# Performance work log

Measured on AMD Instinct MI355X. Metric: run time of the kernel, lower is better.

## Reference

```python
import jax, jax.numpy as jnp
import numpy as np

N_CRYST = 256   # number of crystals
A = 64          # atoms per crystal (uniform)
K = 20          # max_neighbors
HID = 128       # hidden_dim (emb_size_atom/edge)
LAT = 256       # latent_dim
NRBF = 128      # radial basis size
NBLK = 3        # interaction blocks
CUTOFF = 6.0    # radius
N_ATOMS = N_CRYST * A
E = N_ATOMS * K


def _lattice(lengths, angles):
    # lengths, angles: (N_cryst, 3); angles in degrees -> (N_cryst, 3, 3) row-vector lattice
    rad = angles * (np.pi / 180.0)
    cos = jnp.cos(rad)
    sg = jnp.sin(rad[:, 2])
    a, b, c = lengths[:, 0], lengths[:, 1], lengths[:, 2]
    cx = c * cos[:, 1]
    cy = c * (cos[:, 0] - cos[:, 1] * cos[:, 2]) / sg
    cz = jnp.sqrt(jnp.maximum(c ** 2 - cx ** 2 - cy ** 2, 1e-8))
    zeros = jnp.zeros_like(a)
    v1 = jnp.stack([a, zeros, zeros], -1)
    v2 = jnp.stack([b * cos[:, 2], b * sg, zeros], -1)
    v3 = jnp.stack([cx, cy, cz], -1)
    return jnp.stack([v1, v2, v3], axis=1)


def setup_inputs() -> dict:
    key = jax.random.key(0)
    ks = jax.random.split(key, 20)
    z = jax.random.normal(ks[0], (N_CRYST, LAT), jnp.float32)
    frac_coords = jax.random.uniform(ks[1], (N_ATOMS, 3), jnp.float32)
    lengths = 5.0 + 10.0 * jax.random.uniform(ks[2], (N_CRYST, 3), jnp.float32)
    angles = 60.0 + 60.0 * jax.random.uniform(ks[3], (N_CRYST, 3), jnp.float32)
    atom_types = jax.random.randint(ks[4], (N_ATOMS,), 1, 101)
    src = jnp.repeat(jnp.arange(N_ATOMS), K)
    dst = (src // A) * A + jax.random.randint(ks[5], (E,), 0, A)

    def w(k, shape, fan):
        return jax.random.normal(k, shape, jnp.float32) / np.sqrt(fan)

    params = dict(
        emb_table=w(ks[6], (101, HID), 1.0),
        W_in=w(ks[7], (HID + LAT, HID), HID + LAT), b_in=jnp.zeros((HID,), jnp.float32),
        W_edge=w(ks[8], (2 * HID + NRBF, HID), 2 * HID + NRBF), b_edge=jnp.zeros((HID,), jnp.float32),
        Wb_rbf=w(ks[9], (NBLK, NRBF, HID), NRBF),
        Wb_msg=w(ks[10], (NBLK, HID, HID), HID), bb_msg=jnp.zeros((NBLK, HID), jnp.float32),
        Wb_atom=w(ks[11], (NBLK, HID, HID), HID), bb_atom=jnp.zeros((NBLK, HID), jnp.float32),
        Wb_upd=w(ks[12], (NBLK, 3 * HID, HID), 3 * HID), bb_upd=jnp.zeros((NBLK, HID), jnp.float32),
        W_force=w(ks[13], (HID, 1), HID), b_force=jnp.zeros((1,), jnp.float32),
        W_fc1=w(ks[14], (HID, HID), HID), b_fc1=jnp.zeros((HID,), jnp.float32),
        W_fc2=w(ks[15], (HID, HID), HID), b_fc2=jnp.zeros((HID,), jnp.float32),
        W_fc3=w(ks[16], (HID, 2), HID), b_fc3=jnp.zeros((2,), jnp.float32),
    )
    return dict(z=z, frac_coords=frac_coords, lengths=lengths, angles=angles,
                atom_types=atom_types, src=src, dst=dst, **params)


def reference(z, frac_coords, lengths, angles,
              emb_table, W_in, b_in, W_edge, b_edge,
              Wb_rbf, Wb_msg, bb_msg, Wb_atom, bb_atom, Wb_upd, bb_upd,
              W_force, b_force, W_fc1, b_fc1, W_fc2, b_fc2, W_fc3, b_fc3,
              atom_types, src, dst):
    batch_idx = jnp.arange(N_ATOMS) // A  # crystal id per atom
    lattice = _lattice(lengths, angles)   # (N_cryst,3,3)
    cart = jnp.einsum('ni,nij->nj', frac_coords, lattice[batch_idx])  # (N_atoms,3)

    dvec = cart[dst] - cart[src]                        # (E,3)
    dist = jnp.sqrt(jnp.sum(dvec * dvec, -1) + 1e-12)    # (E,)
    unit = dvec / dist[:, None]

    mu = jnp.linspace(0.0, CUTOFF, NRBF)
    delta = CUTOFF / (NRBF - 1)
    env = 0.5 * (jnp.cos(np.pi * jnp.minimum(dist / CUTOFF, 1.0)) + 1.0)  # smooth cutoff
    rbf = jnp.exp(-(((dist[:, None] - mu) / delta) ** 2)) * env[:, None]   # (E,NRBF)

    # atom embedding conditioned on per-crystal latent
    h = jax.nn.relu(jnp.concatenate([emb_table[atom_types], z[batch_idx]], -1) @ W_in + b_in)
    # edge embedding
    m = jax.nn.relu(jnp.concatenate([h[src], h[dst], rbf], -1) @ W_edge + b_edge)

    for i in range(NBLK):
        gate = rbf @ Wb_rbf[i]                                   # (E,HID)
        msg = jax.nn.relu(m @ Wb_msg[i] + bb_msg[i]) * gate       # (E,HID)
        agg = jax.ops.segment_sum(msg, dst, num_segments=N_ATOMS) # (N_atoms,HID)
        h = h + jax.nn.relu(agg @ Wb_atom[i] + bb_atom[i])
        m = m + jax.nn.relu(jnp.concatenate([h[src], h[dst], m], -1) @ Wb_upd[i] + bb_upd[i])

    # per-edge force magnitude projected along edge direction, summed per atom
    f = m @ W_force + b_force                                     # (E,1)
    pred_cart_coord_diff = jax.ops.segment_sum(f * unit, dst, num_segments=N_ATOMS)  # (N_atoms,3)

    a1 = jax.nn.relu(h @ W_fc1 + b_fc1)
    a2 = jax.nn.relu(a1 @ W_fc2 + b_fc2)
    pred_atom_types = a2 @ W_fc3 + b_fc3                          # (N_atoms,2)
    return pred_cart_coord_diff, pred_atom_types
```

## Files before the change

kernel.cpp:

```cpp
#include <hip/hip_runtime.h>
#include <hip/hip_bf16.h>

#define NCRYST 256
#define AATOMS 64
#define KNBR   20
#define HID    128
#define LAT    256
#define NRBF   128
#define NBLK   3
#define NATOMS (NCRYST * AATOMS)
#define NEDGE  (NATOMS * KNBR)
#define NPART  8
#define DQ     4096
#define PI_F   3.14159265358979323846f
#define CUT_F  6.0f
#define CHB    1040
#define EUPGRID 512

typedef short short8 __attribute__((ext_vector_type(8)));
typedef float f32x4  __attribute__((ext_vector_type(4)));

__device__ __forceinline__ float bf2f(__hip_bfloat16 x) { return __bfloat162float(x); }
__device__ __forceinline__ __hip_bfloat16 f2bf(float x) { return __float2bfloat16(x); }
__device__ __forceinline__ float s2f(short x) {
  return __uint_as_float(((unsigned)(unsigned short)x) << 16);
}
__device__ __forceinline__ short f2s(float x) {
  union { short s; __hip_bfloat16 b; } u; u.b = f2bf(x); return u.s;
}

#define DMA16(gptr, lptr) __builtin_amdgcn_global_load_lds( \
    (const __attribute__((address_space(1))) void*)(gptr),  \
    (__attribute__((address_space(3))) void*)(lptr), 16, 0, 0)

#define WCNT_VM11_LGKM0 0x007B
#define WCNT_VM10_LGKM0 0x007A
#define WCNT_VM4_LGKM0  0x0074
#define WCNT_VM0_LGKM0  0x0070
#define WCNT_LGKM0_ONLY 0xC07F

__global__ void k_cart(const float* __restrict__ frac, const float* __restrict__ lengths,
                       const float* __restrict__ angles, float* __restrict__ cart) {
  int atom = blockIdx.x * blockDim.x + threadIdx.x;
  if (atom >= NATOMS) return;
  int c = atom >> 6;
  float al = angles[c*3+0] * (PI_F/180.f);
  float be = angles[c*3+1] * (PI_F/180.f);
  float ga = angles[c*3+2] * (PI_F/180.f);
  float ca = cosf(al), cb = cosf(be), cg = cosf(ga), sg = sinf(ga);
  float a = lengths[c*3+0], b = lengths[c*3+1], cl = lengths[c*3+2];
  float cx = cl * cb;
  float cy = cl * (ca - cb*cg) / sg;
  float cz = sqrtf(fmaxf(cl*cl - cx*cx - cy*cy, 1e-8f));
  float f0 = frac[atom*3+0], f1 = frac[atom*3+1], f2 = frac[atom*3+2];
  cart[atom*3+0] = f0*a + f1*(b*cg) + f2*cx;
  cart[atom*3+1] = f1*(b*sg) + f2*cy;
  cart[atom*3+2] = f2*cz;
}

__global__ void k_edge(const float* __restrict__ cart, const int* __restrict__ src,
                       const int* __restrict__ dst, float* __restrict__ unit,
                       float* __restrict__ dist, const float* __restrict__ b_force,
                       float* __restrict__ fbuf) {
  int e = blockIdx.x * blockDim.x + threadIdx.x;
  if (e >= NEDGE) return;
  int s = src[e], d = dst[e];
  float dx = cart[d*3+0] - cart[s*3+0];
  float dy = cart[d*3+1] - cart[s*3+1];
  float dz = cart[d*3+2] - cart[s*3+2];
  float dd = sqrtf(dx*dx + dy*dy + dz*dz + 1e-12f);
  float inv = 1.f / dd;
  dist[e] = dd;
  unit[e*3+0] = dx*inv; unit[e*3+1] = dy*inv; unit[e*3+2] = dz*inv;
  fbuf[e] = b_force[0];
}

__global__ __launch_bounds__(128) void k_tab(const float* __restrict__ W_edge,
                                             const float* __restrict__ Wb_rbf,
                                             float* __restrict__ T) {
  int q = blockIdx.x, n = threadIdx.x;
  __shared__ float rv[128];
  float d = (float)q * (CUT_F / (float)(DQ - 1));
  float env = 0.5f * (cosf(PI_F * fminf(d * (1.f/CUT_F), 1.f)) + 1.f);
  float t = (d - (float)n * (CUT_F/(NRBF-1))) * ((NRBF-1)/CUT_F);
  rv[n] = expf(-t*t) * env;
  __syncthreads();
  float a0 = 0.f, a1 = 0.f, a2 = 0.f, a3 = 0.f;
  for (int j = 0; j < 128; ++j) {
    float r = rv[j];
    a0 = fmaf(r, W_edge[(256 + j)*128 + n], a0);
    a1 = fmaf(r, Wb_rbf[0*16384 + j*128 + n], a1);
    a2 = fmaf(r, Wb_rbf[1*16384 + j*128 + n], a2);
    a3 = fmaf(r, Wb_rbf[2*16384 + j*128 + n], a3);
  }
  T[(0*DQ + q)*128 + n] = a0;
  T[(1*DQ + q)*128 + n] = a1;
  T[(2*DQ + q)*128 + n] = a2;
  T[(3*DQ + q)*128 + n] = a3;
}

__global__ void k_wcast(const float* __restrict__ W_in, const float* __restrict__ W_edge,
                        const float* __restrict__ Wb_upd, const float* __restrict__ Wb_msg,
                        const float* __restrict__ Wb_atom, const float* __restrict__ W_fc1,
                        const float* __restrict__ W_fc2, __hip_bfloat16* __restrict__ WT) {
  int idx = blockIdx.x * 256 + threadIdx.x;
  if (idx >= 360448) return;
  if (idx < 49152) {
    int n = idx / 384, k = idx % 384;
    WT[idx] = f2bf(W_in[k*128 + n]);
    return;
  }
  int t = idx - 49152;
  int b = t >> 14, q = t & 16383;
  int n = q >> 7, k = q & 127;
  const float* S; int krow;
  if (b == 0)       { S = W_edge; krow = k; }
  else if (b == 1)  { S = W_edge; krow = 128 + k; }
  else if (b <= 10) { int i = (b-2)/3, part = (b-2)%3;
                      S = Wb_upd + i*49152; krow = part*128 + k; }
  else if (b <= 13) { S = Wb_msg + (b-11)*16384; krow = k; }
  else if (b <= 16) { S = Wb_atom + (b-14)*16384; krow = k; }
  else if (b == 17) { S = W_fc1; krow = k; }
  else              { S = W_fc2; krow = k; }
  WT[idx] = f2bf(S[krow*128 + n]);
}

__global__ __launch_bounds__(256) void k_hm(
    const int* __restrict__ atype, const float* __restrict__ z,
    const float* __restrict__ emb, const __hip_bfloat16* __restrict__ WTin,
    const float* __restrict__ b, float* __restrict__ h,
    __hip_bfloat16* __restrict__ h_bf) {
  const int tid = threadIdx.x;
  const int w = tid >> 6, lane = tid & 63, ln = lane & 15, qd = lane >> 4;
  const int row0w = blockIdx.x * 64 + w * 16;
  const int arow = row0w + ln;
  const float* esrc = emb + (size_t)atype[arow] * 128;
  const float* zsrc = z + (size_t)(arow >> 6) * LAT;

  short8 af[12];
#pragma unroll
  for (int ks = 0; ks < 4; ++ks) {
    float4 v0 = *(const float4*)(esrc + ks*32 + qd*8);
    float4 v1 = *(const float4*)(esrc + ks*32 + qd*8 + 4);
    af[ks] = (short8){f2s(v0.x),f2s(v0.y),f2s(v0.z),f2s(v0.w),
                      f2s(v1.x),f2s(v1.y),f2s(v1.z),f2s(v1.w)};
  }
#pragma unroll
  for (int ks = 4; ks < 12; ++ks) {
    float4 v0 = *(const float4*)(zsrc + (ks-4)*32 + qd*8);
    float4 v1 = *(const float4*)(zsrc + (ks-4)*32 + qd*8 + 4);
    af[ks] = (short8){f2s(v0.x),f2s(v0.y),f2s(v0.z),f2s(v0.w),
                      f2s(v1.x),f2s(v1.y),f2s(v1.z),f2s(v1.w)};
  }

  const short* Wb = (const short*)WTin + ln*384 + qd*8;
  f32x4 acc[8];
#pragma unroll
  for (int ct = 0; ct < 8; ++ct) acc[ct] = (f32x4){0,0,0,0};
#pragma unroll
  for (int ks = 0; ks < 12; ++ks)
#pragma unroll
    for (int ct = 0; ct < 8; ++ct)
      acc[ct] = __builtin_amdgcn_mfma_f32_16x16x32_bf16(af[ks],
                  *(const short8*)(Wb + ct*16*384 + ks*32), acc[ct], 0,0,0);

#pragma unroll
  for (int ct = 0; ct < 8; ++ct) {
    int col = ct*16 + ln;
    float bias = b[col];
#pragma unroll
    for (int reg = 0; reg < 4; ++reg) {
      int crow = row0w + qd*4 + reg;
      float v = fmaxf(acc[ct][reg] + bias, 0.f);
      size_t o = (size_t)crow*128 + col;
      h[o] = v;
      h_bf[o] = f2bf(v);
    }
  }
}

__global__ __launch_bounds__(256) void k_uv2(
    const __hip_bfloat16* __restrict__ A,
    const __hip_bfloat16* __restrict__ WT1, const __hip_bfloat16* __restrict__ WT2,
    __hip_bfloat16* __restrict__ O1, __hip_bfloat16* __restrict__ O2) {
  const int tid = threadIdx.x;
  const int w = tid >> 6, lane = tid & 63, ln = lane & 15, qd = lane >> 4;
  const int row0w = blockIdx.x * 64 + w * 16;
  const int arow = row0w + ln;

  short8 af[4];
  const short* pa = (const short*)A + (size_t)arow*128 + qd*8;
#pragma unroll
  for (int ks = 0; ks < 4; ++ks) af[ks] = *(const short8*)(pa + ks*32);

  f32x4 a1[8], a2[8];
#pragma unroll
  for (int ct = 0; ct < 8; ++ct) { a1[ct] = (f32x4){0,0,0,0}; a2[ct] = (f32x4){0,0,0,0}; }
#pragma unroll
  for (int ct = 0; ct < 8; ++ct) {
    const short* b1 = (const short*)WT1 + (ct*16 + ln)*128 + qd*8;
    const short* b2 = (const short*)WT2 + (ct*16 + ln)*128 + qd*8;
#pragma unroll
    for (int ks = 0; ks < 4; ++ks) {
      a1[ct] = __builtin_amdgcn_mfma_f32_16x16x32_bf16(af[ks], *(const short8*)(b1 + ks*32), a1[ct], 0,0,0);
      a2[ct] = __builtin_amdgcn_mfma_f32_16x16x32_bf16(af[ks], *(const short8*)(b2 + ks*32), a2[ct], 0,0,0);
    }
  }
#pragma unroll
  for (int ct = 0; ct < 8; ++ct) {
    int col = ct*16 + ln;
#pragma unroll
    for (int reg = 0; reg < 4; ++reg) {
      size_t o = (size_t)(row0w + qd*4 + reg)*128 + col;
      O1[o] = f2bf(a1[ct][reg]);
      O2[o] = f2bf(a2[ct][reg]);
    }
  }
}

__global__ __launch_bounds__(256) void k_minit(
    const int* __restrict__ src, const int* __restrict__ dst,
    const float* __restrict__ dist,
    const __hip_bfloat16* __restrict__ u0, const __hip_bfloat16* __restrict__ v0,
    const float* __restrict__ T0, const float* __restrict__ b,
    __hip_bfloat16* __restrict__ m) {
  const int t = threadIdx.x;
  const int li = t & 15, ei = t >> 4;
  float bcol[8];
#pragma unroll
  for (int u = 0; u < 8; ++u) bcol[u] = b[li*8 + u];

  int e[4]; float dd[4]; short8 us[4], vs[4];
#pragma unroll
  for (int g = 0; g < 4; ++g) {
    e[g] = blockIdx.x*64 + g*16 + ei;
    dd[g] = dist[e[g]];
    int s = src[e[g]], d = dst[e[g]];
    us[g] = *(const short8*)((const short*)u0 + (size_t)s*128 + li*8);
    vs[g] = *(const short8*)((const short*)v0 + (size_t)d*128 + li*8);
  }
  float t0v[4][8], t1v[4][8]; float fr[4]; bool in[4];
#pragma unroll
  for (int g = 0; g < 4; ++g) {
    in[g] = dd[g] < CUT_F;
    float x = fminf(dd[g], CUT_F) * ((float)(DQ - 1) / CUT_F);
    int i0 = (int)x;
    fr[g] = x - (float)i0;
    const float* tp = T0 + (size_t)i0*128 + li*8;
    *(float4*)&t0v[g][0] = *(const float4*)tp;
    *(float4*)&t0v[g][4] = *(const float4*)(tp + 4);
    *(float4*)&t1v[g][0] = *(const float4*)(tp + 128);
    *(float4*)&t1v[g][4] = *(const float4*)(tp + 132);
  }
#pragma unroll
  for (int g = 0; g < 4; ++g) {
    short8 o;
#pragma unroll
    for (int u = 0; u < 8; ++u) {
      float tv = in[g] ? fmaf(fr[g], t1v[g][u] - t0v[g][u], t0v[g][u]) : 0.f;
      float v = s2f(us[g][u]) + s2f(vs[g][u]) + tv + bcol[u];
      o[u] = f2s(fmaxf(v, 0.f));
    }
    *(uint4*)((short*)m + (size_t)e[g]*128 + li*8) = *(uint4*)&o;
  }
}

template<int MODE>
__global__ __launch_bounds__(256) void k_eup(
    const int* __restrict__ src, const int* __restrict__ dst,
    __hip_bfloat16* __restrict__ m,
    const __hip_bfloat16* __restrict__ uu, const __hip_bfloat16* __restrict__ vv,
    const __hip_bfloat16* __restrict__ WTmm, const float* __restrict__ b,
    const float* __restrict__ Wf, float* __restrict__ fout) {
  __shared__ short Bs[128 * 132];
  __shared__ __align__(16) char Abuf[2][17 * CHB];
  const int tid = threadIdx.x;
  const int w = tid >> 6, lane = tid & 63, ln = lane & 15, qd = lane >> 4;
  const int cg = w & 1, rh = w >> 1;
  const int e_loc = lane >> 4;
  const int sgc = (lane & 15) ^ (e_loc << 2);
  const int NT = NEDGE / 64;

#pragma unroll
  for (int i = 0; i < 8; ++i) {
    int g = i * 256 + tid;
    int colb = g >> 4, ch = g & 15;
    *(uint4*)&Bs[colb*132 + ch*8] = ((const uint4*)((const short*)WTmm + colb*128))[ch];
  }

  float bias4[4], wf4[4];
#pragma unroll
  for (int ct = 0; ct < 4; ++ct) bias4[ct] = b[cg*64 + ct*16 + ln];
  if constexpr (MODE == 2) {
#pragma unroll
    for (int ct = 0; ct < 4; ++ct) wf4[ct] = Wf[cg*64 + ct*16 + ln];
  }

  {
    int tile = blockIdx.x;
#pragma unroll
    for (int t4 = 0; t4 < 4; ++t4) {
      int chunk = w * 4 + t4;
      const short* gp = (const short*)m + (size_t)(tile*64 + chunk*4 + e_loc)*128 + sgc*8;
      DMA16(gp, Abuf[0] + chunk * CHB);
    }
  }

  int it = 0;
  for (int tile = blockIdx.x; tile < NT; tile += EUPGRID, ++it) {
    const int nb = it & 1;
    int ntile = tile + EUPGRID;
    if (ntile < NT) {
#pragma unroll
      for (int t4 = 0; t4 < 4; ++t4) {
        int chunk = w * 4 + t4;
        const short* gp = (const short*)m + (size_t)(ntile*64 + chunk*4 + e_loc)*128 + sgc*8;
        DMA16(gp, Abuf[nb^1] + chunk * CHB);
      }
      __builtin_amdgcn_s_waitcnt(WCNT_VM4_LGKM0);
    } else {
      __builtin_amdgcn_s_waitcnt(WCNT_VM0_LGKM0);
    }
    __builtin_amdgcn_s_barrier();

    const char* Ab = Abuf[nb];
    int e0 = tile * 64;

    f32x4 acc0[4], acc1[4];
#pragma unroll
    for (int ct = 0; ct < 4; ++ct) { acc0[ct] = (f32x4){0,0,0,0}; acc1[ct] = (f32x4){0,0,0,0}; }
    const int rowA = rh*32 + ln, rowB = rowA + 16;
    const int sx = (ln & 3) << 2;
#pragma unroll
    for (int ks = 0; ks < 4; ++ks) {
      int slot = ((ks*4 + qd) ^ sx) << 4;
      short8 aA = *(const short8*)(Ab + (rowA>>2)*CHB + (ln&3)*256 + slot);
      short8 aB = *(const short8*)(Ab + (rowB>>2)*CHB + (ln&3)*256 + slot);
#pragma unroll
      for (int ct = 0; ct < 4; ++ct) {
        short8 bb = *(const short8*)&Bs[(cg*64 + ct*16 + ln)*132 + ks*32 + qd*8];
        acc0[ct] = __builtin_amdgcn_mfma_f32_16x16x32_bf16(aA, bb, acc0[ct], 0,0,0);
        acc1[ct] = __builtin_amdgcn_mfma_f32_16x16x32_bf16(aB, bb, acc1[ct], 0,0,0);
      }
    }

    float vreg[2][4][4];
#pragma unroll
    for (int mt = 0; mt < 2; ++mt) {
      const f32x4* acc = mt ? acc1 : acc0;
#pragma unroll
      for (int reg = 0; reg < 4; ++reg) {
        int lrow = rh*32 + mt*16 + qd*4 + reg;
        int e = e0 + lrow;
        int srow = src[e], drow = dst[e];
        float fp = 0.f;
#pragma unroll
        for (int ct = 0; ct < 4; ++ct) {
          int col = cg*64 + ct*16 + ln;
          float um = s2f(*((const short*)uu + (size_t)srow*128 + col));
          float vm = s2f(*((const short*)vv + (size_t)drow*128 + col));
          int colg = col >> 3;
          float res = s2f(*(const short*)(Ab + (lrow>>2)*CHB + (lrow&3)*256
                         + ((colg ^ ((lrow&3)<<2)) << 4) + (col&7)*2));
          float val = fmaxf(acc[ct][reg] + bias4[ct] + um + vm, 0.f) + res;
          if constexpr (MODE == 1) vreg[mt][reg][ct] = val;
          else fp = fmaf(val, wf4[ct], fp);
        }
        if constexpr (MODE == 2) {
          fp += __shfl_xor(fp, 1, 64);
          fp += __shfl_xor(fp, 2, 64);
          fp += __shfl_xor(fp, 4, 64);
          fp += __shfl_xor(fp, 8, 64);
          if (ln == 0) atomicAdd(&fout[e], fp);
        }
      }
    }

    if constexpr (MODE == 1) {
      __builtin_amdgcn_s_waitcnt(WCNT_LGKM0_ONLY);
      __builtin_amdgcn_s_barrier();
      short* res = (short*)Abuf[nb];
#pragma unroll
      for (int mt = 0; mt < 2; ++mt)
#pragma unroll
        for (int reg = 0; reg < 4; ++reg) {
          int lrow = rh*32 + mt*16 + qd*4 + reg;
#pragma unroll
          for (int ct = 0; ct < 4; ++ct)
            res[lrow*136 + cg*64 + ct*16 + ln] = f2s(vreg[mt][reg][ct]);
        }
      __builtin_amdgcn_s_waitcnt(WCNT_LGKM0_ONLY);
      __builtin_amdgcn_s_barrier();
#pragma unroll
      for (int i = 0; i < 4; ++i) {
        int g = i * 256 + tid;
        int row = g >> 4, ch = g & 15;
        *(uint4*)((short*)m + (size_t)(e0 + row)*128 + ch*8) =
            *(const uint4*)((const char*)Abuf[nb] + row*272 + ch*16);
      }
      __builtin_amdgcn_s_waitcnt(WCNT_LGKM0_ONLY);
      __builtin_amdgcn_s_barrier();
    } else {
      __builtin_amdgcn_s_waitcnt(WCNT_LGKM0_ONLY);
      __builtin_amdgcn_s_barrier();
    }
  }
}

__global__ __launch_bounds__(256, 3) void k_msgagg(
    const __hip_bfloat16* __restrict__ m, const float* __restrict__ dist,
    const __hip_bfloat16* __restrict__ WmT, const float* __restrict__ bm,
    const float* __restrict__ Tg, const int* __restrict__ dst,
    __hip_bfloat16* __restrict__ aggP) {
  __shared__ float gate[32 * 132];
  __shared__ __align__(16) char Mb[2][8 * CHB];
  __shared__ short Pt[128 * 40];
  __shared__ int dstS[160];
  const int tid = threadIdx.x;
  const int c  = blockIdx.x & 255, pq = blockIdx.x >> 8;
  const int w = tid >> 6, lane = tid & 63, ln = lane & 15, qd = lane >> 4;
  const int ei = tid >> 3, li = tid & 7;
  const int e_loc = lane >> 4;
  const int sgc = (lane & 15) ^ (e_loc << 2);
  const int sw8 = (ln & 3) << 3;

  const int ebase = c * 1280 + pq * 160;

  int dv_pre = 0;
  if (tid < 160) dv_pre = dst[ebase + tid] & 63;

  float bias2[2];
#pragma unroll
  for (int ct = 0; ct < 2; ++ct) bias2[ct] = bm[w*32 + ct*16 + ln];

  short8 Bf[2][4];
#pragma unroll
  for (int ct = 0; ct < 2; ++ct) {
    const short* bp = (const short*)WmT + (size_t)(w*32 + ct*16 + ln)*128 + qd*8;
#pragma unroll
    for (int ks = 0; ks < 4; ++ks) Bf[ct][ks] = *(const short8*)(bp + ks*32);
  }

  float4 ta[4], tb[4]; float frc, msk;
  {
    float d0 = dist[ebase + ei];
    msk = (d0 < CUT_F) ? 1.f : 0.f;
    float x = fminf(d0, CUT_F) * ((float)(DQ - 1) / CUT_F);
    int i0 = (int)x; if (i0 > DQ-2) i0 = DQ-2;
    frc = x - (float)i0;
    const float* tp = Tg + (size_t)i0*128 + li*16;
#pragma unroll
    for (int j = 0; j < 4; ++j) {
      ta[j] = *(const float4*)(tp + j*4);
      tb[j] = *(const float4*)(tp + 128 + j*4);
    }
  }
  float dn = dist[ebase + 32 + ei];
#pragma unroll
  for (int t = 0; t < 2; ++t) {
    int chunk = w*2 + t;
    const short* gp = (const short*)m + (size_t)(ebase + chunk*4 + e_loc)*128 + sgc*8;
    DMA16(gp, Mb[0] + chunk*CHB);
  }
#pragma unroll
  for (int j = 0; j < 4; ++j) {
    float4 g;
    g.x = msk * fmaf(frc, tb[j].x - ta[j].x, ta[j].x);
    g.y = msk * fmaf(frc, tb[j].y - ta[j].y, ta[j].y);
    g.z = msk * fmaf(frc, tb[j].z - ta[j].z, ta[j].z);
    g.w = msk * fmaf(frc, tb[j].w - ta[j].w, ta[j].w);
    *(float4*)&gate[ei*132 + li*16 + j*4] = g;
  }
  if (tid < 160) dstS[tid] = dv_pre;
  __builtin_amdgcn_s_waitcnt(WCNT_LGKM0_ONLY);
  __builtin_amdgcn_s_barrier();

  f32x4 accA[4][2];
#pragma unroll
  for (int rt = 0; rt < 4; ++rt)
#pragma unroll
    for (int ct = 0; ct < 2; ++ct) accA[rt][ct] = (f32x4){0,0,0,0};

  for (int s = 0; s < 5; ++s) {
    const int e0 = ebase + s*32;

    if (s < 4) {
      msk = (dn < CUT_F) ? 1.f : 0.f;
      float x = fminf(dn, CUT_F) * ((float)(DQ - 1) / CUT_F);
      int i0 = (int)x; if (i0 > DQ-2) i0 = DQ-2;
      frc = x - (float)i0;
      const float* tp = Tg + (size_t)i0*128 + li*16;
#pragma unroll
      for (int j = 0; j < 4; ++j) {
        ta[j] = *(const float4*)(tp + j*4);
        tb[j] = *(const float4*)(tp + 128 + j*4);
      }
#pragma unroll
      for (int t = 0; t < 2; ++t) {
        int chunk = w*2 + t;
        const short* gp = (const short*)m + (size_t)(e0 + 32 + chunk*4 + e_loc)*128 + sgc*8;
        DMA16(gp, Mb[(s+1) & 1] + chunk*CHB);
      }
      if (s < 3) {
        dn = dist[e0 + 64 + ei];
        __builtin_amdgcn_s_waitcnt(WCNT_VM11_LGKM0);
      } else {
        __builtin_amdgcn_s_waitcnt(WCNT_VM10_LGKM0);
      }
    } else {
      __builtin_amdgcn_s_waitcnt(WCNT_VM0_LGKM0);
    }
    __builtin_amdgcn_s_barrier();

    const char* Ms = Mb[s & 1];
    short8 am[2][4];
#pragma unroll
    for (int et = 0; et < 2; ++et) {
      int r = et*16 + ln;
      const char* rp = Ms + (r>>2)*CHB + (r&3)*256;
      const int sx = (r & 3) << 2;
#pragma unroll
      for (int ks = 0; ks < 4; ++ks)
        am[et][ks] = *(const short8*)(rp + (((ks*4 + qd) ^ sx) << 4));
    }

    f32x4 acc[2][2];
#pragma unroll
    for (int et = 0; et < 2; ++et)
#pragma unroll
      for (int ct = 0; ct < 2; ++ct) acc[et][ct] = (f32x4){0,0,0,0};
#pragma unroll
    for (int ks = 0; ks < 4; ++ks)
#pragma unroll
      for (int et = 0; et < 2; ++et)
#pragma unroll
        for (int ct = 0; ct < 2; ++ct)
          acc[et][ct] = __builtin_amdgcn_mfma_f32_16x16x32_bf16(
              am[et][ks], Bf[ct][ks], acc[et][ct], 0,0,0);

#pragma unroll
    for (int et = 0; et < 2; ++et)
#pragma unroll
      for (int ct = 0; ct < 2; ++ct) {
        const int col = w*32 + ct*16 + ln;
        float p[4];
#pragma unroll
        for (int reg = 0; reg < 4; ++reg) {
          const int erow = et*16 + qd*4 + reg;
          p[reg] = fmaxf(acc[et][ct][reg] + bias2[ct], 0.f) * gate[erow*132 + col];
        }
        unsigned u01 = (unsigned)(unsigned short)f2s(p[0]) |
                       ((unsigned)(unsigned short)f2s(p[1]) << 16);
        unsigned u23 = (unsigned)(unsigned short)f2s(p[2]) |
                       ((unsigned)(unsigned short)f2s(p[3]) << 16);
        const int a0 = col*40 + ((et*16 + qd*4) ^ sw8);
        *(unsigned*)&Pt[a0]     = u01;
        *(unsigned*)&Pt[a0 + 2] = u23;
      }
    __builtin_amdgcn_s_waitcnt(WCNT_LGKM0_ONLY);
    __builtin_amdgcn_s_barrier();

    int dvj[8];
#pragma unroll
    for (int j = 0; j < 8; ++j) dvj[j] = dstS[s*32 + qd*8 + j];
    short8 pb0 = *(const short8*)&Pt[(w*32 + 0*16 + ln)*40 + ((qd*8) ^ sw8)];
    short8 pb1 = *(const short8*)&Pt[(w*32 + 1*16 + ln)*40 + ((qd*8) ^ sw8)];
#pragma unroll
    for (int rt = 0; rt < 4; ++rt) {
      short8 oh;
#pragma unroll
      for (int j = 0; j < 8; ++j)
        oh[j] = (dvj[j] == rt*16 + ln) ? (short)0x3F80 : (short)0;
      accA[rt][0] = __builtin_amdgcn_mfma_f32_16x16x32_bf16(oh, pb0, accA[rt][0], 0,0,0);
      accA[rt][1] = __builtin_amdgcn_mfma_f32_16x16x32_bf16(oh, pb1, accA[rt][1], 0,0,0);
    }

    if (s < 4) {
#pragma unroll
      for (int j = 0; j < 4; ++j) {
        float4 g;
        g.x = msk * fmaf(frc, tb[j].x - ta[j].x, ta[j].x);
        g.y = msk * fmaf(frc, tb[j].y - ta[j].y, ta[j].y);
        g.z = msk * fmaf(frc, tb[j].z - ta[j].z, ta[j].z);
        g.w = msk * fmaf(frc, tb[j].w - ta[j].w, ta[j].w);
        *(float4*)&gate[ei*132 + li*16 + j*4] = g;
      }
    }
  }

  __hip_bfloat16* outp = aggP + ((size_t)pq * NATOMS + c * 64) * HID;
#pragma unroll
  for (int rt = 0; rt < 4; ++rt)
#pragma unroll
    for (int ct = 0; ct < 2; ++ct) {
      const int col = w*32 + ct*16 + ln;
#pragma unroll
      for (int reg = 0; reg < 4; ++reg) {
        const int row = rt*16 + qd*4 + reg;
        outp[(size_t)row*HID + col] = f2bf(accA[rt][ct][reg]);
      }
    }
}

__global__ __launch_bounds__(256) void k_fcuv(
    const __hip_bfloat16* __restrict__ slices,
    const __hip_bfloat16* __restrict__ WTa, const float* __restrict__ ba,
    float* __restrict__ h, __hip_bfloat16* __restrict__ h_bf,
    const __hip_bfloat16* __restrict__ WTu, const __hip_bfloat16* __restrict__ WTv,
    __hip_bfloat16* __restrict__ uo, __hip_bfloat16* __restrict__ vo) {
  __shared__ short ht[64 * 136];
  const int tid = threadIdx.x;
  const int w = tid >> 6, lane = tid & 63, ln = lane & 15, qd = lane >> 4;
  const int row0w = blockIdx.x * 64 + w * 16;
  const int arow = row0w + ln;

  short8 af[4];
#pragma unroll
  for (int ks = 0; ks < 4; ++ks) {
    float s[8] = {0,0,0,0,0,0,0,0};
#pragma unroll
    for (int p = 0; p < NPART; ++p) {
      short8 v = *(const short8*)((const short*)slices +
                   (size_t)p*NATOMS*128 + (size_t)arow*128 + qd*8 + ks*32);
#pragma unroll
      for (int u = 0; u < 8; ++u) s[u] += s2f(v[u]);
    }
    af[ks] = (short8){f2s(s[0]),f2s(s[1]),f2s(s[2]),f2s(s[3]),
                      f2s(s[4]),f2s(s[5]),f2s(s[6]),f2s(s[7])};
  }

  const short* Wb = (const short*)WTa + ln*128 + qd*8;
  f32x4 acc[8];
#pragma unroll
  for (int ct = 0; ct < 8; ++ct) acc[ct] = (f32x4){0,0,0,0};
#pragma unroll
  for (int ct = 0; ct < 8; ++ct)
#pragma unroll
    for (int ks = 0; ks < 4; ++ks)
      acc[ct] = __builtin_amdgcn_mfma_f32_16x16x32_bf16(af[ks],
                  *(const short8*)(Wb + ct*16*128 + ks*32), acc[ct], 0,0,0);

#pragma unroll
  for (int ct = 0; ct < 8; ++ct) {
    int col = ct*16 + ln;
    float bias = ba[col];
#pragma unroll
    for (int reg = 0; reg < 4; ++reg) {
      int lrow = w*16 + qd*4 + reg;
      size_t o = (size_t)(blockIdx.x*64 + lrow)*128 + col;
      float v = fmaxf(acc[ct][reg] + bias, 0.f) + h[o];
      h[o] = v;
      short hb = f2s(v);
      h_bf[o] = *(__hip_bfloat16*)&hb;
      ht[lrow*136 + col] = hb;
    }
  }
  __syncthreads();

  short8 ah[4];
  const short* ph = &ht[(w*16 + ln)*136 + qd*8];
#pragma unroll
  for (int ks = 0; ks < 4; ++ks) ah[ks] = *(const short8*)(ph + ks*32);

  f32x4 a1[8], a2[8];
#pragma unroll
  for (int ct = 0; ct < 8; ++ct) { a1[ct] = (f32x4){0,0,0,0}; a2[ct] = (f32x4){0,0,0,0}; }
#pragma unroll
  for (int ct = 0; ct < 8; ++ct) {
    const short* b1 = (const short*)WTu + (ct*16 + ln)*128 + qd*8;
    const short* b2 = (const short*)WTv + (ct*16 + ln)*128 + qd*8;
#pragma unroll
    for (int ks = 0; ks < 4; ++ks) {
      a1[ct] = __builtin_amdgcn_mfma_f32_16x16x32_bf16(ah[ks], *(const short8*)(b1 + ks*32), a1[ct], 0,0,0);
      a2[ct] = __builtin_amdgcn_mfma_f32_16x16x32_bf16(ah[ks], *(const short8*)(b2 + ks*32), a2[ct], 0,0,0);
    }
  }
#pragma unroll
  for (int ct = 0; ct < 8; ++ct) {
    int col = ct*16 + ln;
#pragma unroll
    for (int reg = 0; reg < 4; ++reg) {
      size_t o = (size_t)(row0w + qd*4 + reg)*128 + col;
      uo[o] = f2bf(a1[ct][reg]);
      vo[o] = f2bf(a2[ct][reg]);
    }
  }
}

__global__ __launch_bounds__(256) void k_head(
    const __hip_bfloat16* __restrict__ h_bf,
    const __hip_bfloat16* __restrict__ WT1, const float* __restrict__ b1,
    const __hip_bfloat16* __restrict__ WT2, const float* __restrict__ b2,
    const float* __restrict__ W3, const float* __restrict__ b3,
    float* __restrict__ out) {
  __shared__ short t1[64 * 136];
  const int tid = threadIdx.x;
  const int w = tid >> 6, lane = tid & 63, ln = lane & 15, qd = lane >> 4;
  const int row0w = blockIdx.x * 64 + w * 16;
  const int arow = row0w + ln;

  short8 af[4];
  const short* pa = (const short*)h_bf + (size_t)arow*128 + qd*8;
#pragma unroll
  for (int ks = 0; ks < 4; ++ks) af[ks] = *(const short8*)(pa + ks*32);

  f32x4 acc[8];
#pragma unroll
  for (int ct = 0; ct < 8; ++ct) acc[ct] = (f32x4){0,0,0,0};
#pragma unroll
  for (int ct = 0; ct < 8; ++ct) {
    const short* bb = (const short*)WT1 + (ct*16 + ln)*128 + qd*8;
#pragma unroll
    for (int ks = 0; ks < 4; ++ks)
      acc[ct] = __builtin_amdgcn_mfma_f32_16x16x32_bf16(af[ks],
                  *(const short8*)(bb + ks*32), acc[ct], 0,0,0);
  }
#pragma unroll
  for (int ct = 0; ct < 8; ++ct) {
    int col = ct*16 + ln;
    float bias = b1[col];
#pragma unroll
    for (int reg = 0; reg < 4; ++reg) {
      int lrow = w*16 + qd*4 + reg;
      t1[lrow*136 + col] = f2s(fmaxf(acc[ct][reg] + bias, 0.f));
    }
  }
  __syncthreads();

  short8 a1f[4];
  const short* p1 = &t1[(w*16 + ln)*136 + qd*8];
#pragma unroll
  for (int ks = 0; ks < 4; ++ks) a1f[ks] = *(const short8*)(p1 + ks*32);

  f32x4 acc2[8];
#pragma unroll
  for (int ct = 0; ct < 8; ++ct) acc2[ct] = (f32x4){0,0,0,0};
#pragma unroll
  for (int ct = 0; ct < 8; ++ct) {
    const short* bb = (const short*)WT2 + (ct*16 + ln)*128 + qd*8;
#pragma unroll
    for (int ks = 0; ks < 4; ++ks)
      acc2[ct] = __builtin_amdgcn_mfma_f32_16x16x32_bf16(a1f[ks],
                   *(const short8*)(bb + ks*32), acc2[ct], 0,0,0);
  }

  float w3a[8], w3b[8];
#pragma unroll
  for (int ct = 0; ct < 8; ++ct) {
    int col = ct*16 + ln;
    w3a[ct] = W3[col*2+0];
    w3b[ct] = W3[col*2+1];
  }
#pragma unroll
  for (int reg = 0; reg < 4; ++reg) {
    float p0 = 0.f, p1v = 0.f;
#pragma unroll
    for (int ct = 0; ct < 8; ++ct) {
      float a2v = fmaxf(acc2[ct][reg] + b2[ct*16 + ln], 0.f);
      p0  = fmaf(a2v, w3a[ct], p0);
      p1v = fmaf(a2v, w3b[ct], p1v);
    }
    p0  += __shfl_xor(p0, 1, 64);  p1v += __shfl_xor(p1v, 1, 64);
    p0  += __shfl_xor(p0, 2, 64);  p1v += __shfl_xor(p1v, 2, 64);
    p0  += __shfl_xor(p0, 4, 64);  p1v += __shfl_xor(p1v, 4, 64);
    p0  += __shfl_xor(p0, 8, 64);  p1v += __shfl_xor(p1v, 8, 64);
    if (ln == 0) {
      int row = row0w + qd*4 + reg;
      out[row*2+0] = p0 + b3[0];
      out[row*2+1] = p1v + b3[1];
    }
  }
}

__global__ void k_pcart(const float* __restrict__ f, const float* __restrict__ unit,
                        const int* __restrict__ dst, float* __restrict__ out) {
  __shared__ float acc[AATOMS * 3];
  int c = blockIdx.x, tid = threadIdx.x;
  if (tid < AATOMS*3) acc[tid] = 0.f;
  __syncthreads();
  for (int t = tid; t < 1280; t += 256) {
    int e = c*1280 + t;
    int d = dst[e] & 63;
    float fv = f[e];
    atomicAdd(&acc[d*3+0], fv * unit[e*3+0]);
    atomicAdd(&acc[d*3+1], fv * unit[e*3+1]);
    atomicAdd(&acc[d*3+2], fv * unit[e*3+2]);
  }
  __syncthreads();
  if (tid < AATOMS*3) out[c*AATOMS*3 + tid] = acc[tid];
}

extern "C" void kernel_launch(void* const* d_in, const int* in_sizes, int n_in,
                              void* d_out, int out_size, void* d_ws, size_t ws_size,
                              hipStream_t stream) {
  const float* z        = (const float*)d_in[0];
  const float* frac     = (const float*)d_in[1];
  const float* lengths  = (const float*)d_in[2];
  const float* angles   = (const float*)d_in[3];
  const int*   atype    = (const int*)  d_in[4];
  const int*   src      = (const int*)  d_in[5];
  const int*   dst      = (const int*)  d_in[6];
  const float* emb      = (const float*)d_in[7];
  const float* W_in     = (const float*)d_in[8];
  const float* b_in     = (const float*)d_in[9];
  const float* W_edge   = (const float*)d_in[10];
  const float* b_edge   = (const float*)d_in[11];
  const float* Wb_rbf   = (const float*)d_in[12];
  const float* Wb_msg   = (const float*)d_in[13];
  const float* bb_msg   = (const float*)d_in[14];
  const float* Wb_atom  = (const float*)d_in[15];
  const float* bb_atom  = (const float*)d_in[16];
  const float* Wb_upd   = (const float*)d_in[17];
  const float* bb_upd   = (const float*)d_in[18];
  const float* W_force  = (const float*)d_in[19];
  const float* b_force  = (const float*)d_in[20];
  const float* W_fc1    = (const float*)d_in[21];
  const float* b_fc1    = (const float*)d_in[22];
  const float* W_fc2    = (const float*)d_in[23];
  const float* b_fc2    = (const float*)d_in[24];
  const float* W_fc3    = (const float*)d_in[25];
  const float* b_fc3    = (const float*)d_in[26];

  char* p = (char*)d_ws;
  float* cart = (float*)p;            p += (size_t)NATOMS*3*4;
  float* unit = (float*)p;            p += (size_t)NEDGE*3*4;
  float* dist = (float*)p;            p += (size_t)NEDGE*4;
  float* h    = (float*)p;            p += (size_t)NATOMS*HID*4;
  float* fbuf = (float*)p;            p += (size_t)NEDGE*4;
  float* T    = (float*)p;            p += (size_t)4*DQ*128*4;
  __hip_bfloat16* h_bf = (__hip_bfloat16*)p; p += (size_t)NATOMS*HID*2;
  __hip_bfloat16* u0t  = (__hip_bfloat16*)p; p += (size_t)NATOMS*HID*2;
  __hip_bfloat16* v0t  = (__hip_bfloat16*)p; p += (size_t)NATOMS*HID*2;
  __hip_bfloat16* uut  = (__hip_bfloat16*)p; p += (size_t)NATOMS*HID*2;
  __hip_bfloat16* vvt  = (__hip_bfloat16*)p; p += (size_t)NATOMS*HID*2;
  __hip_bfloat16* aggP = (__hip_bfloat16*)p; p += (size_t)NPART*NATOMS*HID*2;
  __hip_bfloat16* m    = (__hip_bfloat16*)p; p += (size_t)NEDGE*HID*2;
  __hip_bfloat16* WT   = (__hip_bfloat16*)p; p += (size_t)360448*2;

  __hip_bfloat16* WT_in   = WT;
  __hip_bfloat16* WTK     = WT + 49152;
  __hip_bfloat16* WT_u0   = WTK + 0*16384;
  __hip_bfloat16* WT_v0   = WTK + 1*16384;
  __hip_bfloat16* WT_updB = WTK + 2*16384;
  __hip_bfloat16* WT_msg  = WTK + 11*16384;
  __hip_bfloat16* WT_atom = WTK + 14*16384;
  __hip_bfloat16* WT_fc1  = WTK + 17*16384;
  __hip_bfloat16* WT_fc2  = WTK + 18*16384;

  float* out_cart = (float*)d_out;
  float* out_at   = out_cart + NATOMS*3;

  k_wcast<<<1408, 256, 0, stream>>>(W_in, W_edge, Wb_upd, Wb_msg, Wb_atom,
                                    W_fc1, W_fc2, WT);
  k_tab<<<DQ, 128, 0, stream>>>(W_edge, Wb_rbf, T);
  k_cart<<<NATOMS/256, 256, 0, stream>>>(frac, lengths, angles, cart);
  k_edge<<<NEDGE/256, 256, 0, stream>>>(cart, src, dst, unit, dist, b_force, fbuf);
  k_hm<<<NATOMS/64, 256, 0, stream>>>(atype, z, emb, WT_in, b_in, h, h_bf);
  k_uv2<<<NATOMS/64, 256, 0, stream>>>(h_bf, WT_u0, WT_v0, u0t, v0t);
  k_minit<<<NEDGE/64, 256, 0, stream>>>(src, dst, dist, u0t, v0t, T, b_edge, m);

  for (int i = 0; i < NBLK; ++i) {
    k_msgagg<<<NCRYST*NPART, 256, 0, stream>>>(m, dist, WT_msg + i*16384,
                                               bb_msg + i*HID, T + (size_t)(1+i)*DQ*128,
                                               dst, aggP);
    k_fcuv<<<NATOMS/64, 256, 0, stream>>>(aggP, WT_atom + i*16384, bb_atom + i*HID,
                                          h, h_bf,
                                          WT_updB + (3*i+0)*16384,
                                          WT_updB + (3*i+1)*16384, uut, vvt);
    if (i < NBLK-1) {
      k_eup<1><<<EUPGRID, 256, 0, stream>>>(src, dst, m, uut, vvt,
                                            WT_updB + (3*i+2)*16384, bb_upd + i*HID,
                                            nullptr, nullptr);
    } else {
      k_eup<2><<<EUPGRID, 256, 0, stream>>>(src, dst, m, uut, vvt,
                                            WT_updB + (3*i+2)*16384, bb_upd + i*HID,
                                            W_force, fbuf);
    }
  }
  k_pcart<<<NCRYST, 256, 0, stream>>>(fbuf, unit, dst, out_cart);
  k_head<<<NATOMS/64, 256, 0, stream>>>(h_bf, WT_fc1, b_fc1, WT_fc2, b_fc2,
                                        W_fc3, b_fc3, out_at);
}
```

Before: 665.8 us.

## Gather per-atom u/v terms via one-hot MFMA with crystal-aligned edge blocks

Each k_eup block now handles half of one crystal's edges (640 edges, 10 tiles). The crystal's 64 rows of uu/vv are preloaded into registers as MFMA B operands, and src/dst local indices are cached in LDS. The per-element scattered global gathers of uu[src] and vv[dst] in the epilogue are replaced by one-hot bf16 MFMAs that accumulate those rows into the accumulator. This removes many uncoalesced global loads, but it adds extra MFMA work, register pressure from the Bu/Bv arrays, and relies on every edge's src and dst being in the same 64-atom crystal.

```diff
diff --git a/kernel.cpp b/kernel.cpp
--- a/kernel.cpp
+++ b/kernel.cpp
@@ -15,7 +15,6 @@
 #define PI_F   3.14159265358979323846f
 #define CUT_F  6.0f
 #define CHB    1040
-#define EUPGRID 512
 
 typedef short short8 __attribute__((ext_vector_type(8)));
 typedef float f32x4  __attribute__((ext_vector_type(4)));
@@ -274,12 +273,15 @@
     const float* __restrict__ Wf, float* __restrict__ fout) {
   __shared__ short Bs[128 * 132];
   __shared__ __align__(16) char Abuf[2][17 * CHB];
+  __shared__ short srcS[640], dstS[640];
   const int tid = threadIdx.x;
   const int w = tid >> 6, lane = tid & 63, ln = lane & 15, qd = lane >> 4;
   const int cg = w & 1, rh = w >> 1;
   const int e_loc = lane >> 4;
   const int sgc = (lane & 15) ^ (e_loc << 2);
-  const int NT = NEDGE / 64;
+  const int cry = blockIdx.x >> 1, half = blockIdx.x & 1;
+  const int ebase = cry * 1280 + half * 640;
+  const int ca = cry * 64;
 
 #pragma unroll
   for (int i = 0; i < 8; ++i) {
@@ -287,6 +289,10 @@
     int colb = g >> 4, ch = g & 15;
     *(uint4*)&Bs[colb*132 + ch*8] = ((const uint4*)((const short*)WTmm + colb*128))[ch];
   }
+  for (int i = tid; i < 640; i += 256) {
+    srcS[i] = (short)(src[ebase + i] & 63);
+    dstS[i] = (short)(dst[ebase + i] & 63);
+  }
 
   float bias4[4], wf4[4];
 #pragma unroll
@@ -296,25 +302,35 @@
     for (int ct = 0; ct < 4; ++ct) wf4[ct] = Wf[cg*64 + ct*16 + ln];
   }
 
-  {
-    int tile = blockIdx.x;
-#pragma unroll
-    for (int t4 = 0; t4 < 4; ++t4) {
-      int chunk = w * 4 + t4;
-      const short* gp = (const short*)m + (size_t)(tile*64 + chunk*4 + e_loc)*128 + sgc*8;
-      DMA16(gp, Abuf[0] + chunk * CHB);
-    }
-  }
-
-  int it = 0;
-  for (int tile = blockIdx.x; tile < NT; tile += EUPGRID, ++it) {
-    const int nb = it & 1;
-    int ntile = tile + EUPGRID;
-    if (ntile < NT) {
+  short8 Bu[2][4], Bv[2][4];
+#pragma unroll
+  for (int ks = 0; ks < 2; ++ks)
+#pragma unroll
+    for (int ct = 0; ct < 4; ++ct) {
+      const int col = cg*64 + ct*16 + ln;
+#pragma unroll
+      for (int j = 0; j < 8; ++j) {
+        const size_t ro = (size_t)(ca + ks*32 + qd*8 + j) * 128 + col;
+        Bu[ks][ct][j] = ((const short*)uu)[ro];
+        Bv[ks][ct][j] = ((const short*)vv)[ro];
+      }
+    }
+
+#pragma unroll
+  for (int t4 = 0; t4 < 4; ++t4) {
+    int chunk = w * 4 + t4;
+    const short* gp = (const short*)m + (size_t)(ebase + chunk*4 + e_loc)*128 + sgc*8;
+    DMA16(gp, Abuf[0] + chunk * CHB);
+  }
+
+  for (int t = 0; t < 10; ++t) {
+    const int nb = t & 1;
+    if (t < 9) {
 #pragma unroll
       for (int t4 = 0; t4 < 4; ++t4) {
         int chunk = w * 4 + t4;
-        const short* gp = (const short*)m + (size_t)(ntile*64 + chunk*4 + e_loc)*128 + sgc*8;
+        const short* gp = (const short*)m +
+            (size_t)(ebase + (t+1)*64 + chunk*4 + e_loc)*128 + sgc*8;
         DMA16(gp, Abuf[nb^1] + chunk * CHB);
       }
       __builtin_amdgcn_s_waitcnt(WCNT_VM4_LGKM0);
@@ -324,12 +340,16 @@
     __builtin_amdgcn_s_barrier();
 
     const char* Ab = Abuf[nb];
-    int e0 = tile * 64;
+    const int e0 = ebase + t*64;
+    const int l0 = t*64;
+
+    const int rowA = rh*32 + ln, rowB = rowA + 16;
+    const int sa = srcS[l0 + rowA], da = dstS[l0 + rowA];
+    const int sb = srcS[l0 + rowB], db = dstS[l0 + rowB];
 
     f32x4 acc0[4], acc1[4];
 #pragma unroll
     for (int ct = 0; ct < 4; ++ct) { acc0[ct] = (f32x4){0,0,0,0}; acc1[ct] = (f32x4){0,0,0,0}; }
-    const int rowA = rh*32 + ln, rowB = rowA + 16;
     const int sx = (ln & 3) << 2;
 #pragma unroll
     for (int ks = 0; ks < 4; ++ks) {
@@ -344,6 +364,26 @@
       }
     }
 
+#pragma unroll
+    for (int ks = 0; ks < 2; ++ks) {
+      short8 ohAu, ohAv, ohBu, ohBv;
+#pragma unroll
+      for (int j = 0; j < 8; ++j) {
+        const int kk = ks*32 + qd*8 + j;
+        ohAu[j] = (sa == kk) ? (short)0x3F80 : (short)0;
+        ohAv[j] = (da == kk) ? (short)0x3F80 : (short)0;
+        ohBu[j] = (sb == kk) ? (short)0x3F80 : (short)0;
+        ohBv[j] = (db == kk) ? (short)0x3F80 : (short)0;
+      }
+#pragma unroll
+      for (int ct = 0; ct < 4; ++ct) {
+        acc0[ct] = __builtin_amdgcn_mfma_f32_16x16x32_bf16(ohAu, Bu[ks][ct], acc0[ct], 0,0,0);
+        acc0[ct] = __builtin_amdgcn_mfma_f32_16x16x32_bf16(ohAv, Bv[ks][ct], acc0[ct], 0,0,0);
+        acc1[ct] = __builtin_amdgcn_mfma_f32_16x16x32_bf16(ohBu, Bu[ks][ct], acc1[ct], 0,0,0);
+        acc1[ct] = __builtin_amdgcn_mfma_f32_16x16x32_bf16(ohBv, Bv[ks][ct], acc1[ct], 0,0,0);
+      }
+    }
+
     float vreg[2][4][4];
 #pragma unroll
     for (int mt = 0; mt < 2; ++mt) {
@@ -351,18 +391,14 @@
 #pragma unroll
       for (int reg = 0; reg < 4; ++reg) {
         int lrow = rh*32 + mt*16 + qd*4 + reg;
-        int e = e0 + lrow;
-        int srow = src[e], drow = dst[e];
         float fp = 0.f;
 #pragma unroll
         for (int ct = 0; ct < 4; ++ct) {
           int col = cg*64 + ct*16 + ln;
-          float um = s2f(*((const short*)uu + (size_t)srow*128 + col));
-          float vm = s2f(*((const short*)vv + (size_t)drow*128 + col));
           int colg = col >> 3;
           float res = s2f(*(const short*)(Ab + (lrow>>2)*CHB + (lrow&3)*256
                          + ((colg ^ ((lrow&3)<<2)) << 4) + (col&7)*2));
-          float val = fmaxf(acc[ct][reg] + bias4[ct] + um + vm, 0.f) + res;
+          float val = fmaxf(acc[ct][reg] + bias4[ct], 0.f) + res;
           if constexpr (MODE == 1) vreg[mt][reg][ct] = val;
           else fp = fmaf(val, wf4[ct], fp);
         }
@@ -371,7 +407,7 @@
           fp += __shfl_xor(fp, 2, 64);
           fp += __shfl_xor(fp, 4, 64);
           fp += __shfl_xor(fp, 8, 64);
-          if (ln == 0) atomicAdd(&fout[e], fp);
+          if (ln == 0) atomicAdd(&fout[e0 + lrow], fp);
         }
       }
     }
@@ -868,13 +904,13 @@
                                           WT_updB + (3*i+0)*16384,
                                           WT_updB + (3*i+1)*16384, uut, vvt);
     if (i < NBLK-1) {
-      k_eup<1><<<EUPGRID, 256, 0, stream>>>(src, dst, m, uut, vvt,
-                                            WT_updB + (3*i+2)*16384, bb_upd + i*HID,
-                                            nullptr, nullptr);
+      k_eup<1><<<NCRYST*2, 256, 0, stream>>>(src, dst, m, uut, vvt,
+                                             WT_updB + (3*i+2)*16384, bb_upd + i*HID,
+                                             nullptr, nullptr);
     } else {
-      k_eup<2><<<EUPGRID, 256, 0, stream>>>(src, dst, m, uut, vvt,
-                                            WT_updB + (3*i+2)*16384, bb_upd + i*HID,
-                                            W_force, fbuf);
+      k_eup<2><<<NCRYST*2, 256, 0, stream>>>(src, dst, m, uut, vvt,
+                                             WT_updB + (3*i+2)*16384, bb_upd + i*HID,
+                                             W_force, fbuf);
     }
   }
   k_pcart<<<NCRYST, 256, 0, stream>>>(fbuf, unit, dst, out_cart);
```

Result: faster. 624.7 us (-6.2%).
